# Optimization experiments

Measured on AMD Instinct MI355X. Metric: run time of the kernel, lower is better.

## Reference

```python
import jax, jax.numpy as jnp
import numpy as np

# ---- module constants (from init_kwargs) ----
NOF_LINKS = 64
NOISE = 1e-3          # gen_para.input_noise_power
DT = 0.01             # gen_para.dt
T_END = 5.12          # t
TXP = 1.0             # gen_para.tx_power
LAM = 1.0
RHO = 1.0

T_ARR = jnp.arange(0.0, T_END, DT, dtype=jnp.float32)   # [T] time grid
POW2T = jnp.power(jnp.float32(2.0), T_ARR)               # 2^t
POW2T_1 = POW2T - 1.0                                    # 2^t - 1
LN2 = jnp.log(jnp.float32(2.0))


def setup_inputs() -> dict:
    key = jax.random.key(0)
    k1, k2 = jax.random.split(key)
    pathloss = jax.random.uniform(k1, (NOF_LINKS, NOF_LINKS), dtype=jnp.float32)
    powers = jax.random.uniform(k2, (16, 20, NOF_LINKS), dtype=jnp.float32)
    return {"pathloss": pathloss, "powers": powers}


def _outage(pathloss, power):
    # power: [B, N, L]; pathloss: [L, L]
    B, N, L = power.shape
    T = T_ARR.shape[0]
    # signal[b,n,i,j] = pathloss[i,j] * power[b,n,i]  (per original expand/permute)
    y_ii = jnp.diagonal(pathloss)[None, None, :] * power              # [B,N,L]
    y_tot = power * jnp.sum(pathloss, axis=1)[None, None, :]          # sum_j signal
    y_ij = y_tot - y_ii
    sinr = y_ii / (y_ij + NOISE)                                      # [B,N,L]

    # block-0 outage CDF over time grid: Q1[b,i,t] = 1 - exp(-(2^t-1) * sinr[b,0,i])
    Q1 = 1.0 - jnp.exp(-POW2T_1[None, None, :] * sinr[:, 0, :, None])  # [B,L,T]

    # per-block pdf kernels for n >= 1 (vectorized over all blocks up front)
    s = sinr[:, 1:, :, None]                                          # [B,N-1,L,1]
    q = jnp.exp(-POW2T_1 * s) * POW2T * s * LN2                       # [B,N-1,L,T]

    def step(Q, qn):
        # Q, qn: [B,L,T]; per-channel grouped cross-correlation (torch conv1d semantics)
        x = Q.reshape(1, B * L, T)
        w = qn.reshape(B * L, 1, T)
        out = jax.lax.conv_general_dilated(
            x, w, window_strides=(1,), padding=[(T - 1, T - 1)],
            feature_group_count=B * L)                                 # [1,B*L,2T-1]
        Qn = out[0, :, :T].reshape(B, L, T) * DT
        return Qn, Qn[:, :, -1]

    q_scan = jnp.moveaxis(q, 1, 0)                                    # [N-1,B,L,T]
    _, outa_rest = jax.lax.scan(step, Q1, q_scan)                     # [N-1,B,L]
    outa = jnp.concatenate([Q1[None, :, :, -1], outa_rest], axis=0)   # [N,B,L]
    return jnp.moveaxis(outa, 0, 1)                                   # [B,N,L]


def reference(pathloss, powers):
    power = powers * TXP
    N = power.shape[1]
    outa = _outage(pathloss, power)                                   # [B,N,L]
    E = power[:, 0, :] + jnp.sum(power[:, 1:, :] * outa[:, :N - 1, :], axis=1)
    D = 1.0 + jnp.sum(outa[:, :N - 1, :], axis=1)
    loss = jnp.sum(E) + LAM * jnp.sum(outa[:, N - 1, :]) + RHO * jnp.sum(D)
    return loss
```

## Files before the change

### kernel.cpp

```cpp
#include <hip/hip_runtime.h>

#define LL 64
#define NN 20
#define DTC 0.01f
#define NOISEC 1e-3f
#define LN2C 0.69314718056f
#define LOG2E 1.44269504089f

typedef __attribute__((ext_vector_type(8))) short short8x;
typedef __attribute__((ext_vector_type(4))) float f32x4;
typedef __attribute__((ext_vector_type(4))) int v4i;

__device__ __forceinline__ unsigned cvt_pk_bf16(float x, float y) {
    unsigned r;
    asm("v_cvt_pk_bf16_f32 %0, %1, %2" : "=v"(r) : "v"(x), "v"(y));
    return r;
}

template<int CTRL>
__device__ __forceinline__ short8x dpp_shr(short8x v) {
    v4i p = __builtin_bit_cast(v4i, v);
    v4i q;
    q.x = __builtin_amdgcn_update_dpp(0, p.x, CTRL, 0xf, 0xf, true);
    q.y = __builtin_amdgcn_update_dpp(0, p.y, CTRL, 0xf, 0xf, true);
    q.z = __builtin_amdgcn_update_dpp(0, p.z, CTRL, 0xf, 0xf, true);
    q.w = __builtin_amdgcn_update_dpp(0, p.w, CTRL, 0xf, 0xf, true);
    return __builtin_bit_cast(short8x, q);
}

__global__ __launch_bounds__(64, 1) void outage_kernel(
    const float* __restrict__ pathloss,
    const float* __restrict__ powers,
    float* __restrict__ out)
{
    __shared__ __align__(16) unsigned short gt[2][8][544];
    __shared__ __align__(16) unsigned short Qb[2][1024];

    const int lane = threadIdx.x;
    const int c = blockIdx.x, b = c >> 6, l = c & 63;
    const int nh = lane & 15;
    const int qd = lane >> 4;

    const float pl = pathloss[l * LL + lane];
    float rs = pl;
    #pragma unroll
    for (int mk = 1; mk < 64; mk <<= 1) rs += __shfl_xor(rs, mk, 64);
    const float dg   = __shfl(pl, l, 64);
    const float dsum = rs - dg;

    float P2[8], P1L[8];
    #pragma unroll
    for (int u = 0; u < 8; ++u) {
        float e = __builtin_amdgcn_exp2f((8 * lane + u) * DTC);
        P2[u]  = e;
        P1L[u] = (1.f - e) * LOG2E;
    }

    *((uint4*)&Qb[0][0] + lane) = uint4{0u, 0u, 0u, 0u};
    *((uint4*)&Qb[1][0] + lane) = uint4{0u, 0u, 0u, 0u};
    {
        const int bb = lane >> 5, w = lane & 31;
        #pragma unroll
        for (int k = 0; k < 8; ++k) gt[bb][k][512 + w] = 0;
    }

    const float p0 = powers[(b * NN + 0) * LL + l];
    const float s0 = dg * p0 / (p0 * dsum + NOISEC);
    float q7;
    {
        float v[8];
        #pragma unroll
        for (int u = 0; u < 8; ++u) v[u] = 1.f - __builtin_amdgcn_exp2f(P1L[u] * s0);
        q7 = v[7];
        uint4 d4 = { cvt_pk_bf16(v[0], v[1]), cvt_pk_bf16(v[2], v[3]),
                     cvt_pk_bf16(v[4], v[5]), cvt_pk_bf16(v[6], v[7]) };
        *(uint4*)&Qb[0][512 + 8 * lane] = d4;
    }

    const float p1v = powers[(b * NN + 1) * LL + l];
    float lossCh = 1.f + p0 + (p1v + 1.f) * q7;

    auto fill_g = [&](int buf, float p) {
        float s  = dg * p / (p * dsum + NOISEC);
        float cm = s * LN2C * DTC;
        unsigned F[8];
        #pragma unroll
        for (int w = 0; w < 4; ++w) {
            float a  = __builtin_amdgcn_exp2f(P1L[2 * w]     * s) * (P2[2 * w]     * cm);
            float bb = __builtin_amdgcn_exp2f(P1L[2 * w + 1] * s) * (P2[2 * w + 1] * cm);
            F[w] = cvt_pk_bf16(a, bb);
        }
        #pragma unroll
        for (int w = 0; w < 4; ++w) {
            unsigned t = (unsigned)__shfl_down((int)F[w], 1, 64);
            F[4 + w] = (lane == 63) ? 0u : t;
        }
        unsigned E[7];
        #pragma unroll
        for (int j = 0; j < 7; ++j) E[j] = (F[j] >> 16) | (F[j + 1] << 16);
        #pragma unroll
        for (int k = 0; k < 8; ++k) {
            uint4 d4;
            if ((k & 1) == 0) d4 = uint4{F[k / 2], F[k / 2 + 1], F[k / 2 + 2], F[k / 2 + 3]};
            else              d4 = uint4{E[k / 2], E[k / 2 + 1], E[k / 2 + 2], E[k / 2 + 3]};
            *(uint4*)&gt[buf][k][8 * lane] = d4;
        }
    };
    fill_g(1, p1v);

    const int kk    = (7 - nh) & 7;
    const int baseA = 511 - nh + 8 * qd - kk;
    const int baseB = 512 + 32 * nh + 8 * qd;
    const int dstw  = 512 + 32 * nh + 4 * qd;

    float pnext = powers[(b * NN + 2) * LL + l];

    for (int n = 1; n < NN; ++n) {
        const unsigned short* psrc = &Qb[(n + 1) & 1][0];
        const unsigned short* pg   = &gt[n & 1][kk][0];
        unsigned short* pdst       = &Qb[n & 1][0];

        float pfut = 0.f;
        if (n <= NN - 3) pfut = powers[(b * NN + n + 2) * LL + l];

        short8x Bv[16];
        Bv[0]  = *(const short8x*)&psrc[baseB];
        Bv[1]  = dpp_shr<0x111>(Bv[0]);
        Bv[2]  = dpp_shr<0x112>(Bv[0]);
        Bv[3]  = dpp_shr<0x113>(Bv[0]);
        Bv[4]  = dpp_shr<0x114>(Bv[0]);
        Bv[5]  = dpp_shr<0x115>(Bv[0]);
        Bv[6]  = dpp_shr<0x116>(Bv[0]);
        Bv[7]  = dpp_shr<0x117>(Bv[0]);
        Bv[8]  = dpp_shr<0x118>(Bv[0]);
        Bv[9]  = dpp_shr<0x119>(Bv[0]);
        Bv[10] = dpp_shr<0x11A>(Bv[0]);
        Bv[11] = dpp_shr<0x11B>(Bv[0]);
        Bv[12] = dpp_shr<0x11C>(Bv[0]);
        Bv[13] = dpp_shr<0x11D>(Bv[0]);
        Bv[14] = dpp_shr<0x11E>(Bv[0]);
        Bv[15] = dpp_shr<0x11F>(Bv[0]);

        short8x A0v[16], A1v[16];
        #pragma unroll
        for (int d = 0; d < 16; ++d) {
            A0v[d] = *(const short8x*)&pg[baseA - 32 * d];
            A1v[d] = *(const short8x*)&pg[baseA - 32 * d - 16];
        }

        if (n < NN - 1) fill_g((n + 1) & 1, pnext);

        f32x4 acc0a = {0.f, 0.f, 0.f, 0.f}, acc0b = {0.f, 0.f, 0.f, 0.f};
        f32x4 acc1a = {0.f, 0.f, 0.f, 0.f}, acc1b = {0.f, 0.f, 0.f, 0.f};
        #pragma unroll
        for (int d = 0; d < 16; d += 2) {
            acc0a = __builtin_amdgcn_mfma_f32_16x16x32_bf16(A0v[d],     Bv[d],     acc0a, 0, 0, 0);
            acc1a = __builtin_amdgcn_mfma_f32_16x16x32_bf16(A1v[d],     Bv[d],     acc1a, 0, 0, 0);
            acc0b = __builtin_amdgcn_mfma_f32_16x16x32_bf16(A0v[d + 1], Bv[d + 1], acc0b, 0, 0, 0);
            acc1b = __builtin_amdgcn_mfma_f32_16x16x32_bf16(A1v[d + 1], Bv[d + 1], acc1b, 0, 0, 0);
        }
        f32x4 acc0 = acc0a + acc0b;
        f32x4 acc1 = acc1a + acc1b;

        *(uint2*)&pdst[dstw]      = uint2{cvt_pk_bf16(acc0.x, acc0.y), cvt_pk_bf16(acc0.z, acc0.w)};
        *(uint2*)&pdst[dstw + 16] = uint2{cvt_pk_bf16(acc1.x, acc1.y), cvt_pk_bf16(acc1.z, acc1.w)};

        float wgt = (n < NN - 1) ? (pnext + 1.f) : 1.f;
        lossCh += wgt * acc1.w;
        pnext = pfut;
    }

    if (lane == 63) atomicAdd(out, lossCh);
}

extern "C" void kernel_launch(void* const* d_in, const int* in_sizes, int n_in,
                              void* d_out, int out_size, void* d_ws, size_t ws_size,
                              hipStream_t stream) {
    const float* pathloss = (const float*)d_in[0];
    const float* powers   = (const float*)d_in[1];
    float* outp = (float*)d_out;

    (void)hipMemsetAsync(d_out, 0, sizeof(float) * out_size, stream);
    outage_kernel<<<16 * LL, 64, 0, stream>>>(pathloss, powers, outp);
}
```

Measured before the change: 85.59 us.

## Split per-channel convolution across two wavefronts with per-step barrier

Each block now runs two wavefronts instead of one. Each wave computes one of the two 16-column output halves of the bf16 MFMA convolution and writes half of the next-step kernel tiles. This halves the per-wave MFMA chain and A-operand loads, which should shorten the serial 19-step recurrence per channel. In exchange it adds a __syncthreads per step and makes both waves redundantly compute the DPP-shifted B operands and the exponentials. A small alignbit substitution also replaces a shift/or pair in the tile packing.

```diff
diff --git a/kernel.cpp b/kernel.cpp
--- a/kernel.cpp
+++ b/kernel.cpp
@@ -28,7 +28,7 @@
     return __builtin_bit_cast(short8x, q);
 }
 
-__global__ __launch_bounds__(64, 1) void outage_kernel(
+__global__ __launch_bounds__(128, 2) void outage_kernel(
     const float* __restrict__ pathloss,
     const float* __restrict__ powers,
     float* __restrict__ out)
@@ -36,7 +36,8 @@
     __shared__ __align__(16) unsigned short gt[2][8][544];
     __shared__ __align__(16) unsigned short Qb[2][1024];
 
-    const int lane = threadIdx.x;
+    const int lane = threadIdx.x & 63;
+    const int wid  = threadIdx.x >> 6;
     const int c = blockIdx.x, b = c >> 6, l = c & 63;
     const int nh = lane & 15;
     const int qd = lane >> 4;
@@ -56,9 +57,10 @@
         P1L[u] = (1.f - e) * LOG2E;
     }
 
-    *((uint4*)&Qb[0][0] + lane) = uint4{0u, 0u, 0u, 0u};
-    *((uint4*)&Qb[1][0] + lane) = uint4{0u, 0u, 0u, 0u};
-    {
+    if (wid == 0) {
+        *((uint4*)&Qb[0][0] + lane) = uint4{0u, 0u, 0u, 0u};
+    } else {
+        *((uint4*)&Qb[1][0] + lane) = uint4{0u, 0u, 0u, 0u};
         const int bb = lane >> 5, w = lane & 31;
         #pragma unroll
         for (int k = 0; k < 8; ++k) gt[bb][k][512 + w] = 0;
@@ -72,9 +74,11 @@
         #pragma unroll
         for (int u = 0; u < 8; ++u) v[u] = 1.f - __builtin_amdgcn_exp2f(P1L[u] * s0);
         q7 = v[7];
-        uint4 d4 = { cvt_pk_bf16(v[0], v[1]), cvt_pk_bf16(v[2], v[3]),
-                     cvt_pk_bf16(v[4], v[5]), cvt_pk_bf16(v[6], v[7]) };
-        *(uint4*)&Qb[0][512 + 8 * lane] = d4;
+        if (wid == 0) {
+            uint4 d4 = { cvt_pk_bf16(v[0], v[1]), cvt_pk_bf16(v[2], v[3]),
+                         cvt_pk_bf16(v[4], v[5]), cvt_pk_bf16(v[6], v[7]) };
+            *(uint4*)&Qb[0][512 + 8 * lane] = d4;
+        }
     }
 
     const float p1v = powers[(b * NN + 1) * LL + l];
@@ -97,23 +101,27 @@
         }
         unsigned E[7];
         #pragma unroll
-        for (int j = 0; j < 7; ++j) E[j] = (F[j] >> 16) | (F[j + 1] << 16);
+        for (int j = 0; j < 7; ++j) E[j] = __builtin_amdgcn_alignbit(F[j + 1], F[j], 16);
         #pragma unroll
-        for (int k = 0; k < 8; ++k) {
+        for (int k = 0; k < 4; ++k) {
+            const int kw = k + 4 * wid;
             uint4 d4;
-            if ((k & 1) == 0) d4 = uint4{F[k / 2], F[k / 2 + 1], F[k / 2 + 2], F[k / 2 + 3]};
-            else              d4 = uint4{E[k / 2], E[k / 2 + 1], E[k / 2 + 2], E[k / 2 + 3]};
-            *(uint4*)&gt[buf][k][8 * lane] = d4;
+            if ((kw & 1) == 0) d4 = uint4{F[kw / 2], F[kw / 2 + 1], F[kw / 2 + 2], F[kw / 2 + 3]};
+            else               d4 = uint4{E[kw / 2], E[kw / 2 + 1], E[kw / 2 + 2], E[kw / 2 + 3]};
+            *(uint4*)&gt[buf][kw][8 * lane] = d4;
         }
     };
     fill_g(1, p1v);
 
     const int kk    = (7 - nh) & 7;
     const int baseA = 511 - nh + 8 * qd - kk;
+    const int aoff  = baseA - (wid << 4);
     const int baseB = 512 + 32 * nh + 8 * qd;
-    const int dstw  = 512 + 32 * nh + 4 * qd;
+    const int dstw  = 512 + 32 * nh + 4 * qd + (wid << 4);
 
     float pnext = powers[(b * NN + 2) * LL + l];
+
+    __syncthreads();
 
     for (int n = 1; n < NN; ++n) {
         const unsigned short* psrc = &Qb[(n + 1) & 1][0];
@@ -141,36 +149,32 @@
         Bv[14] = dpp_shr<0x11E>(Bv[0]);
         Bv[15] = dpp_shr<0x11F>(Bv[0]);
 
-        short8x A0v[16], A1v[16];
+        short8x Av[16];
         #pragma unroll
-        for (int d = 0; d < 16; ++d) {
-            A0v[d] = *(const short8x*)&pg[baseA - 32 * d];
-            A1v[d] = *(const short8x*)&pg[baseA - 32 * d - 16];
-        }
+        for (int d = 0; d < 16; ++d) Av[d] = *(const short8x*)&pg[aoff - 32 * d];
 
         if (n < NN - 1) fill_g((n + 1) & 1, pnext);
 
-        f32x4 acc0a = {0.f, 0.f, 0.f, 0.f}, acc0b = {0.f, 0.f, 0.f, 0.f};
-        f32x4 acc1a = {0.f, 0.f, 0.f, 0.f}, acc1b = {0.f, 0.f, 0.f, 0.f};
+        f32x4 accA = {0.f, 0.f, 0.f, 0.f}, accB = {0.f, 0.f, 0.f, 0.f};
         #pragma unroll
         for (int d = 0; d < 16; d += 2) {
-            acc0a = __builtin_amdgcn_mfma_f32_16x16x32_bf16(A0v[d],     Bv[d],     acc0a, 0, 0, 0);
-            acc1a = __builtin_amdgcn_mfma_f32_16x16x32_bf16(A1v[d],     Bv[d],     acc1a, 0, 0, 0);
-            acc0b = __builtin_amdgcn_mfma_f32_16x16x32_bf16(A0v[d + 1], Bv[d + 1], acc0b, 0, 0, 0);
-            acc1b = __builtin_amdgcn_mfma_f32_16x16x32_bf16(A1v[d + 1], Bv[d + 1], acc1b, 0, 0, 0);
+            accA = __builtin_amdgcn_mfma_f32_16x16x32_bf16(Av[d],     Bv[d],     accA, 0, 0, 0);
+            accB = __builtin_amdgcn_mfma_f32_16x16x32_bf16(Av[d + 1], Bv[d + 1], accB, 0, 0, 0);
         }
-        f32x4 acc0 = acc0a + acc0b;
-        f32x4 acc1 = acc1a + acc1b;
+        f32x4 acc = accA + accB;
 
-        *(uint2*)&pdst[dstw]      = uint2{cvt_pk_bf16(acc0.x, acc0.y), cvt_pk_bf16(acc0.z, acc0.w)};
-        *(uint2*)&pdst[dstw + 16] = uint2{cvt_pk_bf16(acc1.x, acc1.y), cvt_pk_bf16(acc1.z, acc1.w)};
+        *(uint2*)&pdst[dstw] = uint2{cvt_pk_bf16(acc.x, acc.y), cvt_pk_bf16(acc.z, acc.w)};
 
-        float wgt = (n < NN - 1) ? (pnext + 1.f) : 1.f;
-        lossCh += wgt * acc1.w;
+        if (wid == 1) {
+            float wgt = (n < NN - 1) ? (pnext + 1.f) : 1.f;
+            lossCh += wgt * acc.w;
+        }
         pnext = pfut;
+
+        __syncthreads();
     }
 
-    if (lane == 63) atomicAdd(out, lossCh);
+    if (wid == 1 && lane == 63) atomicAdd(out, lossCh);
 }
 
 extern "C" void kernel_launch(void* const* d_in, const int* in_sizes, int n_in,
@@ -181,5 +185,5 @@
     float* outp = (float*)d_out;
 
     (void)hipMemsetAsync(d_out, 0, sizeof(float) * out_size, stream);
-    outage_kernel<<<16 * LL, 64, 0, stream>>>(pathloss, powers, outp);
+    outage_kernel<<<16 * LL, 128, 0, stream>>>(pathloss, powers, outp);
 }
```

New measurement: 95.82 us. +12.0%, slower.
